# Kernel optimization log

Hardware: AMD Instinct MI355X
Metric: run time of the kernel (lower is better)

The kernel has to match this reference:

```python
import jax, jax.numpy as jnp
import numpy as np

B, S, D, H = 2, 2048, 1024, 16
HD = D // H  # head_dim = 64


def setup_inputs() -> dict:
    key = jax.random.key(0)
    k1, k2, k3 = jax.random.split(key, 3)
    x = jax.random.normal(k1, (B, S, D), dtype=jnp.float32)
    W_qkv = jax.random.normal(k2, (D, 3 * D), dtype=jnp.float32) * (D ** -0.5)
    b_qkv = jnp.zeros((3 * D,), dtype=jnp.float32)
    W_proj = jax.random.normal(k3, (D, D), dtype=jnp.float32) * (D ** -0.5)
    b_proj = jnp.zeros((D,), dtype=jnp.float32)
    return {"x": x, "W_qkv": W_qkv, "b_qkv": b_qkv, "W_proj": W_proj, "b_proj": b_proj}


def reference(x, W_qkv, b_qkv, W_proj, b_proj):
    b, s, d = x.shape
    scale = HD ** -0.5
    qkv = x @ W_qkv + b_qkv                       # [B,S,3D]
    q, k, v = jnp.split(qkv, 3, axis=-1)
    # [B,S,D] -> [B,H,S,HD]
    def to_heads(t):
        return t.reshape(b, s, H, HD).transpose(0, 2, 1, 3)
    q, k, v = map(to_heads, (q, k, v))
    scores = jnp.einsum('bhqd,bhkd->bhqk', q, k) * scale  # [B,H,S,S]
    causal = jnp.triu(jnp.ones((s, s), dtype=bool), k=1)
    scores = jnp.where(causal[None, None], -jnp.inf, scores)
    attn = jax.nn.softmax(scores, axis=-1)
    out = jnp.einsum('bhqk,bhkd->bhqd', attn, v)  # [B,H,S,HD]
    out = out.transpose(0, 2, 1, 3).reshape(b, s, d)
    return out @ W_proj + b_proj
```

## Files before the change

### kernel.cpp

```cpp
#include <hip/hip_runtime.h>

using frag_t = __attribute__((ext_vector_type(8))) short;
using f32x4  = __attribute__((ext_vector_type(4))) float;

#define L2E 1.4426950408889634f

constexpr int B_  = 2, S_ = 2048, D_ = 1024, H_ = 16, HD_ = 64;
constexpr int M_  = B_ * S_;
constexpr float QSCALE = 0.125f * L2E;

__device__ __forceinline__ ushort f2bf(float f) {
  union { float f; unsigned u; } v; v.f = f;
  unsigned u = v.u;
  unsigned r = (u + 0x7FFFu + ((u >> 16) & 1u)) >> 16;
  return (ushort)r;
}
__device__ __forceinline__ ushort f2bf_fast(float f) {
  union { float f; unsigned u; } v; v.f = f;
  return (ushort)((v.u + 0x8000u) >> 16);
}

__device__ __forceinline__ void gld_lds16(const ushort* g, ushort* l) {
  __builtin_amdgcn_global_load_lds((const __attribute__((address_space(1))) void*)g,
                                   (__attribute__((address_space(3))) void*)l, 16, 0, 0);
}

__global__ __launch_bounds__(256) void k_prep(
    const float* __restrict__ x, const float* __restrict__ Wqkv,
    const float* __restrict__ Wproj,
    ushort* __restrict__ Xbf, ushort* __restrict__ Wqt, ushort* __restrict__ Wpt) {
  int blk = blockIdx.x, tid = threadIdx.x;
  if (blk < 1024) {
    size_t base = (size_t)blk * 4096 + tid * 4;
    #pragma unroll
    for (int i = 0; i < 4; ++i) {
      float4 f = *(const float4*)(x + base + i * 1024);
      ushort4 o;
      o.x = f2bf(f.x); o.y = f2bf(f.y); o.z = f2bf(f.z); o.w = f2bf(f.w);
      *(ushort4*)(Xbf + base + i * 1024) = o;
    }
  } else {
    __shared__ float tile[64][65];
    const float* in; ushort* out; int N, K, bx, by;
    if (blk < 1024 + 768) { int b2 = blk - 1024; in = Wqkv;  out = Wqt; N = 3072; K = 1024; bx = b2 % 48; by = b2 / 48; }
    else                  { int b2 = blk - 1792; in = Wproj; out = Wpt; N = 1024; K = 1024; bx = b2 % 16; by = b2 / 16; }
    int n0 = bx * 64, k0 = by * 64;
    int tx = tid & 63, ty = tid >> 6;
    #pragma unroll
    for (int i = 0; i < 16; ++i)
      tile[ty + i * 4][tx] = in[(size_t)(k0 + ty + i * 4) * N + n0 + tx];
    __syncthreads();
    #pragma unroll
    for (int i = 0; i < 16; ++i)
      out[(size_t)(n0 + ty + i * 4) * K + k0 + tx] = f2bf(tile[tx][ty + i * 4]);
  }
}

template <int EPI>
__global__ __launch_bounds__(256) void k_gemm(
    const ushort* __restrict__ A, const ushort* __restrict__ Bt,
    const float* __restrict__ bias,
    ushort* __restrict__ Qo, ushort* __restrict__ Ko, ushort* __restrict__ Vo,
    float* __restrict__ Co, int N, int K) {
  constexpr int BM = (EPI == 0) ? 128 : 64;
  constexpr int BN = 128, BK = 32;
  constexpr int MI = 4, NI = (EPI == 0) ? 4 : 2;
  constexpr int NDMA = (EPI == 0) ? 4 : 3;
  __shared__ ushort As[3][BM * BK];
  __shared__ ushort Bs[3][BN * BK];
  int tid  = threadIdx.x;
  int lane = tid & 63, wave = tid >> 6;
  int quad = lane >> 4, li = lane & 15;
  int m0 = blockIdx.y * BM, n0 = blockIdx.x * BN;
  int srow   = lane >> 2;
  int gchunk = (lane & 3) ^ (srow & 3) ^ ((lane >> 4) & 3);
  int rsl    = (li ^ (li >> 2)) & 3;
  int mbase  = (EPI == 0) ? (wave >> 1) * 64 : 0;
  int nbase  = (EPI == 0) ? (wave & 1) * 64 : wave * 32;
  int niter  = K / BK;

  auto stage = [&](int it, int b) {
    int k0 = it * BK;
    if (EPI == 0) {
      #pragma unroll
      for (int i = 0; i < 2; ++i) {
        int rbase = wave * 32 + i * 16;
        gld_lds16(&A [(size_t)(m0 + rbase + srow) * K + k0 + gchunk * 8], &As[b][rbase * BK]);
        gld_lds16(&Bt[(size_t)(n0 + rbase + srow) * K + k0 + gchunk * 8], &Bs[b][rbase * BK]);
      }
    } else {
      int ra = wave * 16;
      gld_lds16(&A[(size_t)(m0 + ra + srow) * K + k0 + gchunk * 8], &As[b][ra * BK]);
      #pragma unroll
      for (int i = 0; i < 2; ++i) {
        int rbase = wave * 32 + i * 16;
        gld_lds16(&Bt[(size_t)(n0 + rbase + srow) * K + k0 + gchunk * 8], &Bs[b][rbase * BK]);
      }
    }
  };

  f32x4 acc[MI][NI] = {};
  stage(0, 0);
  stage(1, 1);
  for (int it = 0; it < niter; ++it) {
    __builtin_amdgcn_s_waitcnt(0x0F70 | NDMA);
    __builtin_amdgcn_s_barrier();
    __builtin_amdgcn_sched_barrier(0);
    int ipre = (it + 2 < niter) ? it + 2 : niter - 1;
    stage(ipre, (it + 2) % 3);
    int b = it % 3;
    frag_t af[MI], bf[NI];
    #pragma unroll
    for (int mi = 0; mi < MI; ++mi)
      af[mi] = *(const frag_t*)&As[b][(mbase + mi * 16 + li) * BK + ((quad ^ rsl) * 8)];
    #pragma unroll
    for (int ni = 0; ni < NI; ++ni)
      bf[ni] = *(const frag_t*)&Bs[b][(nbase + ni * 16 + li) * BK + ((quad ^ rsl) * 8)];
    #pragma unroll
    for (int mi = 0; mi < MI; ++mi)
      #pragma unroll
      for (int ni = 0; ni < NI; ++ni)
        acc[mi][ni] = __builtin_amdgcn_mfma_f32_16x16x32_bf16(af[mi], bf[ni], acc[mi][ni], 0, 0, 0);
  }
  __syncthreads();

  if (EPI == 1) {
    #pragma unroll
    for (int mi = 0; mi < MI; ++mi)
      #pragma unroll
      for (int ni = 0; ni < NI; ++ni) {
        int gcol = n0 + nbase + ni * 16 + li;
        float bv = bias[gcol];
        #pragma unroll
        for (int r = 0; r < 4; ++r) {
          int grow = m0 + mbase + mi * 16 + quad * 4 + r;
          Co[(size_t)grow * N + gcol] = acc[mi][ni][r] + bv;
        }
      }
  } else {
    int which = (n0 + nbase) >> 10;
    if (which < 2) {
      #pragma unroll
      for (int mi = 0; mi < MI; ++mi)
        #pragma unroll
        for (int ni = 0; ni < NI; ++ni) {
          int gcol = n0 + nbase + ni * 16 + li;
          float bv = bias[gcol];
          #pragma unroll
          for (int r = 0; r < 4; ++r) {
            int grow = m0 + mbase + mi * 16 + quad * 4 + r;
            float v = acc[mi][ni][r] + bv;
            int d = gcol & 1023, h = d >> 6, hd = d & 63;
            int b = grow >> 11, s = grow & 2047;
            size_t bh = (size_t)b * H_ + h;
            if (which == 0) Qo[(bh * S_ + s) * HD_ + hd] = f2bf(v * QSCALE);
            else            Ko[(bh * S_ + s) * HD_ + hd] = f2bf(v);
          }
        }
    } else {
      ushort* vlds = ((ushort*)As) + wave * (64 * 72);
      #pragma unroll
      for (int ni = 0; ni < NI; ++ni) {
        float bv = bias[n0 + nbase + ni * 16 + li];
        #pragma unroll
        for (int mi = 0; mi < MI; ++mi)
          #pragma unroll
          for (int r = 0; r < 4; ++r)
            vlds[(ni * 16 + li) * 72 + mi * 16 + quad * 4 + r] = f2bf(acc[mi][ni][r] + bv);
      }
      int hgrp = ((n0 & 1023) + nbase) >> 6;
      int b = m0 >> 11;
      int s0 = (m0 & 2047) + mbase;
      size_t vbase = (size_t)(b * H_ + hgrp) * HD_ * S_;
      #pragma unroll
      for (int i = 0; i < 8; ++i) {
        int row = i * 8 + (lane >> 3);
        int col = (lane & 7) * 8;
        *(uint4*)&Vo[vbase + (size_t)row * S_ + s0 + col] = *(const uint4*)&vlds[row * 72 + col];
      }
    }
  }
}

__global__ __launch_bounds__(256) void k_attn(
    const ushort* __restrict__ Q, const ushort* __restrict__ K,
    const ushort* __restrict__ Vt, ushort* __restrict__ O) {
  __shared__ ushort Kbuf[2][64 * 64];
  __shared__ ushort Vbuf[2][64 * 64];
  __shared__ ushort Plds[4 * 16 * 64];
  int lane = threadIdx.x & 63, wave = threadIdx.x >> 6;
  int quad = lane >> 4, li = lane & 15;
  int bh = blockIdx.x;
  int qb = 31 - (int)blockIdx.y;
  int b = bh >> 4, h = bh & 15;
  int q0 = qb * 64 + wave * 16;
  const ushort* Qb = Q  + (size_t)bh * S_ * HD_;
  const ushort* Kb = K  + (size_t)bh * S_ * HD_;
  const ushort* Vb = Vt + (size_t)bh * HD_ * S_;
  ushort* Pw = &Plds[wave * 1024];

  frag_t qf[2];
  #pragma unroll
  for (int ks = 0; ks < 2; ++ks)
    qf[ks] = *(const frag_t*)&Qb[(size_t)(q0 + li) * HD_ + ks * 32 + quad * 8];

  f32x4 o[4] = {};
  float l_r[4] = {0.f, 0.f, 0.f, 0.f};

  auto stage = [&](int kb, int bi) {
    #pragma unroll
    for (int i = 0; i < 2; ++i) {
      int rt  = wave * 16 + i * 8 + (lane >> 3);
      int c16 = (lane & 7) ^ (lane >> 3);
      gld_lds16(&Kb[(size_t)(kb * 64 + rt) * HD_ + c16 * 8], &Kbuf[bi][(wave * 16 + i * 8) * 64]);
      gld_lds16(&Vb[(size_t)rt * S_ + kb * 64 + c16 * 8],    &Vbuf[bi][(wave * 16 + i * 8) * 64]);
    }
  };

  auto comp = [&](int kb, bool diag, int bi) {
    f32x4 sc[4];
    #pragma unroll
    for (int t = 0; t < 4; ++t) {
      f32x4 a = {};
      #pragma unroll
      for (int ks = 0; ks < 2; ++ks) {
        frag_t kf = *(const frag_t*)&Kbuf[bi][(t * 16 + li) * 64 + (((quad + ks * 4) ^ (li & 7)) * 8)];
        a = __builtin_amdgcn_mfma_f32_16x16x32_bf16(qf[ks], kf, a, 0, 0, 0);
      }
      sc[t] = a;
    }
    if (diag) {
      #pragma unroll
      for (int t = 0; t < 4; ++t) {
        int key = kb * 64 + t * 16 + li;
        #pragma unroll
        for (int r = 0; r < 4; ++r)
          if (key > q0 + quad * 4 + r) sc[t][r] = -1e30f;
      }
    }
    #pragma unroll
    for (int t = 0; t < 4; ++t)
      #pragma unroll
      for (int r = 0; r < 4; ++r) {
        float p = exp2f(sc[t][r]);
        l_r[r] += p;
        int row = quad * 4 + r;
        int swr = ((row >> 2) << 1) | (row & 1);
        Pw[row * 64 + (((t * 2 + (li >> 3)) ^ swr) * 8) + (li & 7)] = f2bf_fast(p);
      }
    frag_t pf[2];
    int swl = ((li >> 2) << 1) | (li & 1);
    #pragma unroll
    for (int ks = 0; ks < 2; ++ks)
      pf[ks] = *(const frag_t*)&Pw[li * 64 + (((ks * 4 + quad) ^ swl) * 8)];
    #pragma unroll
    for (int t = 0; t < 4; ++t)
      #pragma unroll
      for (int ks = 0; ks < 2; ++ks) {
        frag_t vf = *(const frag_t*)&Vbuf[bi][(t * 16 + li) * 64 + (((quad + ks * 4) ^ (li & 7)) * 8)];
        o[t] = __builtin_amdgcn_mfma_f32_16x16x32_bf16(pf[ks], vf, o[t], 0, 0, 0);
      }
  };

  stage(0, 0);
  __syncthreads();
  for (int kb = 0; kb <= qb; ++kb) {
    if (kb < qb) stage(kb + 1, (kb + 1) & 1);
    comp(kb, kb == qb, kb & 1);
    __syncthreads();
  }

  #pragma unroll
  for (int r = 0; r < 4; ++r) {
    float t = l_r[r];
    #pragma unroll
    for (int off = 1; off < 16; off <<= 1) t += __shfl_xor(t, off);
    float inv = 1.f / t;
    int srow = q0 + quad * 4 + r;
    #pragma unroll
    for (int ht = 0; ht < 4; ++ht)
      O[((size_t)b * S_ + srow) * D_ + h * 64 + ht * 16 + li] = f2bf(o[ht][r] * inv);
  }
}

extern "C" void kernel_launch(void* const* d_in, const int* in_sizes, int n_in,
                              void* d_out, int out_size, void* d_ws, size_t ws_size,
                              hipStream_t stream) {
  (void)in_sizes; (void)n_in; (void)out_size; (void)ws_size;
  const float* x     = (const float*)d_in[0];
  const float* Wqkv  = (const float*)d_in[1];
  const float* bqkv  = (const float*)d_in[2];
  const float* Wproj = (const float*)d_in[3];
  const float* bproj = (const float*)d_in[4];
  float* out = (float*)d_out;

  char* ws = (char*)d_ws;
  ushort* Xbf = (ushort*)(ws);
  ushort* Wqt = (ushort*)(ws + (8u  << 20));
  ushort* Wpt = (ushort*)(ws + (14u << 20));
  ushort* Qbf = (ushort*)(ws + (16u << 20));
  ushort* Kbf = (ushort*)(ws + (24u << 20));
  ushort* Vtb = (ushort*)(ws + (32u << 20));
  ushort* Obf = Xbf;

  k_prep<<<dim3(2048), dim3(256), 0, stream>>>(x, Wqkv, Wproj, Xbf, Wqt, Wpt);
  k_gemm<0><<<dim3(24, 32), dim3(256), 0, stream>>>(Xbf, Wqt, bqkv, Qbf, Kbf, Vtb,
                                                    (float*)nullptr, 3 * D_, D_);
  k_attn<<<dim3(B_ * H_, 32), dim3(256), 0, stream>>>(Qbf, Kbf, Vtb, Obf);
  k_gemm<1><<<dim3(8, 64), dim3(256), 0, stream>>>(Obf, Wpt, bproj,
                                                   (ushort*)nullptr, (ushort*)nullptr, (ushort*)nullptr,
                                                   out, D_, D_);
}
```

Measured before the change: 194.7 us.

## Rework GEMM pipeline to register-staged double buffering with BK=64

Replaces the triple-buffered direct global-to-LDS loads with register-staged loads (global to VGPR, then written to LDS) using two LDS buffers, and doubles BK to 64 so each barrier pair covers two MFMA k-steps. The output-projection GEMM now uses a 2x2 wave layout instead of 1x4, and the LDS swizzle changes to an 8-chunk XOR pattern. The goal is fewer barriers per unit of work and better load/compute overlap. In exchange it uses more registers and issues two __syncthreads per iteration, and it gives up the asynchronous LDS DMA path.

```diff
diff --git a/kernel.cpp b/kernel.cpp
--- a/kernel.cpp
+++ b/kernel.cpp
@@ -63,66 +63,68 @@
     ushort* __restrict__ Qo, ushort* __restrict__ Ko, ushort* __restrict__ Vo,
     float* __restrict__ Co, int N, int K) {
   constexpr int BM = (EPI == 0) ? 128 : 64;
-  constexpr int BN = 128, BK = 32;
-  constexpr int MI = 4, NI = (EPI == 0) ? 4 : 2;
-  constexpr int NDMA = (EPI == 0) ? 4 : 3;
-  __shared__ ushort As[3][BM * BK];
-  __shared__ ushort Bs[3][BN * BK];
+  constexpr int BN = 128, BK = 64;
+  constexpr int MI = (EPI == 0) ? 4 : 2, NI = 4;
+  constexpr int ANI = BM / 32;
+  __shared__ ushort smem[2 * (BM + BN) * BK];
+  ushort* As = smem;
+  ushort* Bs = smem + 2 * BM * BK;
   int tid  = threadIdx.x;
   int lane = tid & 63, wave = tid >> 6;
   int quad = lane >> 4, li = lane & 15;
+  int wy = wave >> 1, wx = wave & 1;
+  int mbase = wy * (MI * 16), nbase = wx * 64;
   int m0 = blockIdx.y * BM, n0 = blockIdx.x * BN;
-  int srow   = lane >> 2;
-  int gchunk = (lane & 3) ^ (srow & 3) ^ ((lane >> 4) & 3);
-  int rsl    = (li ^ (li >> 2)) & 3;
-  int mbase  = (EPI == 0) ? (wave >> 1) * 64 : 0;
-  int nbase  = (EPI == 0) ? (wave & 1) * 64 : wave * 32;
-  int niter  = K / BK;
-
-  auto stage = [&](int it, int b) {
+  int srow = lane >> 3, sch = lane & 7;
+  int wch  = (sch ^ srow) * 8;
+  int niter = K / BK;
+
+  uint4 ar[ANI], br[4];
+  auto gload = [&](int it) {
     int k0 = it * BK;
-    if (EPI == 0) {
-      #pragma unroll
-      for (int i = 0; i < 2; ++i) {
-        int rbase = wave * 32 + i * 16;
-        gld_lds16(&A [(size_t)(m0 + rbase + srow) * K + k0 + gchunk * 8], &As[b][rbase * BK]);
-        gld_lds16(&Bt[(size_t)(n0 + rbase + srow) * K + k0 + gchunk * 8], &Bs[b][rbase * BK]);
-      }
-    } else {
-      int ra = wave * 16;
-      gld_lds16(&A[(size_t)(m0 + ra + srow) * K + k0 + gchunk * 8], &As[b][ra * BK]);
-      #pragma unroll
-      for (int i = 0; i < 2; ++i) {
-        int rbase = wave * 32 + i * 16;
-        gld_lds16(&Bt[(size_t)(n0 + rbase + srow) * K + k0 + gchunk * 8], &Bs[b][rbase * BK]);
-      }
-    }
+    #pragma unroll
+    for (int i = 0; i < ANI; ++i)
+      ar[i] = *(const uint4*)&A[(size_t)(m0 + i * 32 + wave * 8 + srow) * K + k0 + sch * 8];
+    #pragma unroll
+    for (int i = 0; i < 4; ++i)
+      br[i] = *(const uint4*)&Bt[(size_t)(n0 + i * 32 + wave * 8 + srow) * K + k0 + sch * 8];
   };
+  auto swrite = [&](int b) {
+    #pragma unroll
+    for (int i = 0; i < ANI; ++i)
+      *(uint4*)&As[(size_t)b * BM * BK + (i * 32 + wave * 8 + srow) * BK + wch] = ar[i];
+    #pragma unroll
+    for (int i = 0; i < 4; ++i)
+      *(uint4*)&Bs[(size_t)b * BN * BK + (i * 32 + wave * 8 + srow) * BK + wch] = br[i];
+  };
 
   f32x4 acc[MI][NI] = {};
-  stage(0, 0);
-  stage(1, 1);
+  gload(0); swrite(0);
+  gload(1);
   for (int it = 0; it < niter; ++it) {
-    __builtin_amdgcn_s_waitcnt(0x0F70 | NDMA);
-    __builtin_amdgcn_s_barrier();
-    __builtin_amdgcn_sched_barrier(0);
-    int ipre = (it + 2 < niter) ? it + 2 : niter - 1;
-    stage(ipre, (it + 2) % 3);
-    int b = it % 3;
-    frag_t af[MI], bf[NI];
-    #pragma unroll
-    for (int mi = 0; mi < MI; ++mi)
-      af[mi] = *(const frag_t*)&As[b][(mbase + mi * 16 + li) * BK + ((quad ^ rsl) * 8)];
-    #pragma unroll
-    for (int ni = 0; ni < NI; ++ni)
-      bf[ni] = *(const frag_t*)&Bs[b][(nbase + ni * 16 + li) * BK + ((quad ^ rsl) * 8)];
-    #pragma unroll
-    for (int mi = 0; mi < MI; ++mi)
+    __syncthreads();
+    int b = it & 1;
+    #pragma unroll
+    for (int ks = 0; ks < 2; ++ks) {
+      frag_t af[MI], bf[NI];
+      #pragma unroll
+      for (int mi = 0; mi < MI; ++mi)
+        af[mi] = *(const frag_t*)&As[(size_t)b * BM * BK + (mbase + mi * 16 + li) * BK + (((ks * 4 + quad) ^ (li & 7)) * 8)];
       #pragma unroll
       for (int ni = 0; ni < NI; ++ni)
-        acc[mi][ni] = __builtin_amdgcn_mfma_f32_16x16x32_bf16(af[mi], bf[ni], acc[mi][ni], 0, 0, 0);
-  }
-  __syncthreads();
+        bf[ni] = *(const frag_t*)&Bs[(size_t)b * BN * BK + (nbase + ni * 16 + li) * BK + (((ks * 4 + quad) ^ (li & 7)) * 8)];
+      #pragma unroll
+      for (int mi = 0; mi < MI; ++mi)
+        #pragma unroll
+        for (int ni = 0; ni < NI; ++ni)
+          acc[mi][ni] = __builtin_amdgcn_mfma_f32_16x16x32_bf16(af[mi], bf[ni], acc[mi][ni], 0, 0, 0);
+    }
+    __syncthreads();
+    if (it + 1 < niter) {
+      swrite((it + 1) & 1);
+      if (it + 2 < niter) gload(it + 2);
+    }
+  }
 
   if (EPI == 1) {
     #pragma unroll
@@ -158,7 +160,8 @@
           }
         }
     } else {
-      ushort* vlds = ((ushort*)As) + wave * (64 * 72);
+      __syncthreads();
+      ushort* vlds = smem + wave * (64 * 72);
       #pragma unroll
       for (int ni = 0; ni < NI; ++ni) {
         float bv = bias[n0 + nbase + ni * 16 + li];
```

After: 270.6 us. +39.0%, slower.
